# Performance work log

Hardware: AMD Instinct MI355X
Metric: run time of the kernel (lower is better)

## Reference

```python
import jax, jax.numpy as jnp
import numpy as np

REG_MAX = 16
TOPK = 13
ALPHA = 1.0
BETA = 6.0
MATCH_W = 0.5
IOU_W = 7.5
DFL_W = 1.5
EPS = 1e-7
NEG_INF = -1e30


def _iou(b1, b2):
    # xyxy IoU, broadcastable [..., 4]
    x1 = jnp.maximum(b1[..., 0], b2[..., 0]); y1 = jnp.maximum(b1[..., 1], b2[..., 1])
    x2 = jnp.minimum(b1[..., 2], b2[..., 2]); y2 = jnp.minimum(b1[..., 3], b2[..., 3])
    inter = jnp.maximum(x2 - x1, 0.0) * jnp.maximum(y2 - y1, 0.0)
    a1 = (b1[..., 2] - b1[..., 0]) * (b1[..., 3] - b1[..., 1])
    a2 = (b2[..., 2] - b2[..., 0]) * (b2[..., 3] - b2[..., 1])
    return inter / (a1 + a2 - inter + EPS)


def _ciou(b1, b2):
    iou = _iou(b1, b2)
    w1 = b1[..., 2] - b1[..., 0]; h1 = b1[..., 3] - b1[..., 1]
    w2 = b2[..., 2] - b2[..., 0]; h2 = b2[..., 3] - b2[..., 1]
    cw = jnp.maximum(b1[..., 2], b2[..., 2]) - jnp.minimum(b1[..., 0], b2[..., 0])
    ch = jnp.maximum(b1[..., 3], b2[..., 3]) - jnp.minimum(b1[..., 1], b2[..., 1])
    c2 = cw * cw + ch * ch + EPS
    rho2 = ((b2[..., 0] + b2[..., 2] - b1[..., 0] - b1[..., 2]) ** 2
            + (b2[..., 1] + b2[..., 3] - b1[..., 1] - b1[..., 3]) ** 2) / 4.0
    v = (4.0 / jnp.pi ** 2) * (jnp.arctan(w2 / (h2 + EPS)) - jnp.arctan(w1 / (h1 + EPS))) ** 2
    a = jax.lax.stop_gradient(v / (v - iou + (1.0 + EPS)))
    return iou - (rho2 / c2 + v * a)


def _per_sample(ps, pb, bd, gtb, gtl, vcm, anchor, stride):
    # ps [N,C], pb [N,4], bd [N,4*R], gtb [M,4], gtl [M], vcm [C] bool
    N, C = ps.shape
    M = gtb.shape[0]
    lab = jnp.clip(gtl, 0, C - 1)
    gt_valid = (gtl >= 0) & (gtl < C) & vcm[lab]
    ax, ay = anchor[:, 0], anchor[:, 1]
    inside = ((ax[None, :] >= gtb[:, 0:1]) & (ax[None, :] <= gtb[:, 2:3])
              & (ay[None, :] >= gtb[:, 1:2]) & (ay[None, :] <= gtb[:, 3:4]))  # [M,N]
    iou_mn = _iou(pb[None, :, :], gtb[:, None, :])                             # [M,N]
    cls_mn = jax.nn.sigmoid(ps[:, lab]).T                                      # [M,N]
    align = jnp.where(inside & gt_valid[:, None], cls_mn ** ALPHA * iou_mn ** BETA, NEG_INF)
    top_vals, top_idx = jax.lax.top_k(align, TOPK)                             # [M,K]
    cand = jnp.full((M, N), NEG_INF, ps.dtype).at[jnp.arange(M)[:, None], top_idx].set(top_vals)
    best = cand.max(0)          # final metric per anchor
    mg = cand.argmax(0)         # winning GT (first max == earliest GT, matching loop order)
    fg = best > -1.0            # align >= 0 always; non-candidates stay at NEG_INF
    m_lab = jnp.clip(gtl[mg], 0, C - 1)
    ov = iou_mn[mg, jnp.arange(N)]
    fgf = fg.astype(ps.dtype)
    tgt_scores = jax.nn.one_hot(m_lab, C, dtype=ps.dtype) * (jnp.maximum(ov, 0.1) * fgf)[:, None]
    tb = jnp.where(fg[:, None], gtb[mg], pb)   # safe target boxes (masked out when not fg)

    # classification BCE over valid classes (mean)
    bce = jnp.maximum(ps, 0.0) - ps * tgt_scores + jnp.log1p(jnp.exp(-jnp.abs(ps)))
    vc = vcm.astype(ps.dtype)
    match = (bce * vc[None, :]).sum() / (N * jnp.maximum(vc.sum(), 1.0))

    cnt = fg.sum()
    ciou_v = _ciou(pb, tb)
    iou_loss = jnp.where(cnt > 0, ((1.0 - ciou_v) * fgf).sum() / jnp.maximum(cnt, 1), 0.0)
    miou_sum = (_iou(pb, tb) * fgf).sum()
    probs = jax.nn.sigmoid(ps)
    pos_sum = (probs[jnp.arange(N), m_lab] * fgf).sum()

    # DFL
    d = jnp.concatenate([anchor - tb[:, :2], tb[:, 2:] - anchor], -1) / stride  # [N,4]
    d = jnp.clip(d, 0.0, REG_MAX - 1 - 0.01)
    tl = d.astype(jnp.int32)
    tr = jnp.minimum(tl + 1, REG_MAX - 1)
    wl = tr.astype(ps.dtype) - d
    wr = 1.0 - wl
    logp = jax.nn.log_softmax(bd.reshape(N, 4, REG_MAX), -1)
    ll = -jnp.take_along_axis(logp, tl[..., None], -1)[..., 0]
    lr = -jnp.take_along_axis(logp, tr[..., None], -1)[..., 0]
    dfl = jnp.where(cnt > 0, ((ll * wl + lr * wr) * fgf[:, None]).sum() / jnp.maximum(cnt * 4, 1), 0.0)

    mx = jnp.where(vcm[None, :], probs, NEG_INF).max(-1)
    neg_sum = (mx * (1.0 - fgf)).sum()
    neg_cnt = N - cnt
    return match, iou_loss, dfl, cnt, neg_cnt, pos_sum, neg_sum, miou_sum


def setup_inputs() -> dict:
    key = jax.random.key(0)
    B, N, C, M, R = 16, 8400, 80, 64, REG_MAX
    ks = jax.random.split(key, 7)
    pts, sts = [], []
    for s in (8, 16, 32):
        n = 640 // s
        g = (np.arange(n) + 0.5) * s
        xv, yv = np.meshgrid(g, g)
        pts.append(np.stack([xv.ravel(), yv.ravel()], 1))
        sts.append(np.full((n * n, 1), s, np.float32))
    anchor_points = jnp.asarray(np.concatenate(pts).astype(np.float32))  # [8400,2]
    stride_tensor = jnp.asarray(np.concatenate(sts))                      # [8400,1]
    c = anchor_points[None] + jax.random.normal(ks[0], (B, N, 2)) * stride_tensor[None]
    wh = jax.random.uniform(ks[1], (B, N, 2), minval=8.0, maxval=128.0)
    pred_boxes = jnp.concatenate([jnp.clip(c - wh / 2, 0.0, 640.0),
                                  jnp.clip(c + wh / 2, 0.0, 640.0)], -1)
    gc = jax.random.uniform(ks[2], (B, M, 2), minval=64.0, maxval=576.0)
    gwh = jax.random.uniform(ks[3], (B, M, 2), minval=16.0, maxval=128.0)
    gt_boxes = jnp.concatenate([gc - gwh / 2, gc + gwh / 2], -1)
    gt_labels = jax.random.randint(ks[4], (B, M), 0, C)
    class_mask = jnp.ones((B, C), bool)
    pred_scores = jax.random.normal(ks[5], (B, N, C))
    box_distribution = jax.random.normal(ks[6], (B, N, 4 * R))
    return {"pred_scores": pred_scores, "pred_boxes": pred_boxes,
            "anchor_points": anchor_points, "stride_tensor": stride_tensor,
            "box_distribution": box_distribution, "gt_boxes": gt_boxes,
            "gt_labels": gt_labels, "class_mask": class_mask}


def reference(pred_scores, pred_boxes, anchor_points, stride_tensor,
              box_distribution, gt_boxes, gt_labels, class_mask):
    B = pred_scores.shape[0]
    f = lambda ps, pb, bd, gtb, gtl, vcm: _per_sample(ps, pb, bd, gtb, gtl, vcm,
                                                      anchor_points, stride_tensor)
    match, iou_l, dfl, cnt, ncnt, psum, nsum, misum = jax.vmap(f)(
        pred_scores, pred_boxes, box_distribution, gt_boxes, gt_labels, class_mask)
    tot_pos = cnt.sum()
    tot_neg = ncnt.sum()
    total_match = match.sum(); total_iou = iou_l.sum(); total_dfl = dfl.sum()
    loss = (MATCH_W * total_match + IOU_W * total_iou + DFL_W * total_dfl) / B
    mean_pos = psum.sum() / jnp.maximum(tot_pos, 1)
    mean_neg = nsum.sum() / jnp.maximum(tot_neg, 1)
    mean_miou = misum.sum() / jnp.maximum(tot_pos, 1)
    return (loss, total_match / B, total_iou / B, total_dfl / B,
            tot_pos.astype(jnp.float32), mean_pos, mean_neg, mean_miou)
```

## Files before the change

kernel.cpp:

```cpp
#include <hip/hip_runtime.h>
#include <stdint.h>

#define TOPK 13
#define NEG_INF_F (-1e30f)
#define EPSF 1e-7f
#define L2EF 1.4426950408889634f
#define LN2F 0.6931471805599453f
#define MAXCAND 2048
#define MAXB_LDS 64

__device__ __forceinline__ int mask_at(const uint8_t* __restrict__ raw, int i) {
    bool as_u8 = (raw[1] | raw[2] | raw[3]) != 0;
    return as_u8 ? (raw[i] != 0) : (((const int*)raw)[i] != 0);
}

__device__ __forceinline__ float iou_pair(float ax1, float ay1, float ax2, float ay2,
                                          float bx1, float by1, float bx2, float by2) {
    float x1 = fmaxf(ax1, bx1), y1 = fmaxf(ay1, by1);
    float x2 = fminf(ax2, bx2), y2 = fminf(ay2, by2);
    float inter = fmaxf(x2 - x1, 0.f) * fmaxf(y2 - y1, 0.f);
    float a1 = (ax2 - ax1) * (ay2 - ay1);
    float a2 = (bx2 - bx1) * (by2 - by1);
    return inter / (a1 + a2 - inter + EPSF);
}

__device__ __forceinline__ float sigmoid_fast(float s) {
    return 1.f / (1.f + exp2f(-s * L2EF));
}
__device__ __forceinline__ float softplus_bce(float s) {
    float t = exp2f(-fabsf(s) * L2EF);
    return fmaxf(s, 0.f) + log2f(1.f + t) * LN2F;
}

__device__ __forceinline__ void assign_wave(
    const float* __restrict__ ps, const float* __restrict__ pb,
    const float* __restrict__ gtb, const int* __restrict__ gtl,
    const uint8_t* __restrict__ mraw,
    unsigned long long* __restrict__ best, unsigned* __restrict__ list,
    int B, int N, int C, int M, int t, int lane) {
    int b = t % B;
    int m = t / B;

    int lbl = gtl[b * M + m];
    int lab = min(max(lbl, 0), C - 1);
    if (!((lbl >= 0) && (lbl < C) && (mask_at(mraw, b * C + lab) != 0))) return;

    float4 g = ((const float4*)gtb)[(size_t)b * M + m];

    const int   n0_[3]  = { 0, 6400, 8000 };
    const int   dim_[3] = { 80, 40, 20 };
    const float sv_[3]  = { 8.f, 16.f, 32.f };

    int ix0[3], iy0[3], ww[3], pre[4];
    pre[0] = 0;
#pragma unroll
    for (int l = 0; l < 3; ++l) {
        float s = sv_[l]; int d = dim_[l];
        int ax0 = max(0,     (int)ceilf (g.x / s - 0.5f));
        int ax1 = min(d - 1, (int)floorf(g.z / s - 0.5f));
        int ay0 = max(0,     (int)ceilf (g.y / s - 0.5f));
        int ay1 = min(d - 1, (int)floorf(g.w / s - 0.5f));
        int w = max(0, ax1 - ax0 + 1);
        int h = max(0, ay1 - ay0 + 1);
        ix0[l] = ax0; iy0[l] = ay0; ww[l] = w;
        pre[l + 1] = pre[l] + w * h;
    }
    int tot = pre[3];
    if (tot == 0) return;

    const float* psb = ps + (size_t)b * N * C + lab;
    const float4* pbb = (const float4*)pb + (size_t)b * N;

    float lv[TOPK];
    int   li[TOPK];
#pragma unroll
    for (int j = 0; j < TOPK; ++j) { lv[j] = NEG_INF_F; li[j] = -1; }

    for (int tt = lane; tt < tot; tt += 64) {
        int l = (tt >= pre[1]) + (tt >= pre[2]);
        int r = tt - pre[l];
        int w = ww[l];
        int iy = r / w, ix = r - iy * w;
        int gx = ix0[l] + ix, gy = iy0[l] + iy;
        int n = n0_[l] + gy * dim_[l] + gx;
        float4 p = pbb[n];
        float iou = iou_pair(p.x, p.y, p.z, p.w, g.x, g.y, g.z, g.w);
        float sc = psb[(size_t)n * C];
        float i3 = iou * iou * iou;
        float val = sigmoid_fast(sc) * i3 * i3;
        if (val > lv[TOPK - 1]) {
            bool placed = false;
#pragma unroll
            for (int j = TOPK - 1; j >= 1; --j) {
                if (!placed) {
                    if (val > lv[j - 1]) { lv[j] = lv[j - 1]; li[j] = li[j - 1]; }
                    else { lv[j] = val; li[j] = n; placed = true; }
                }
            }
            if (!placed) { lv[0] = val; li[0] = n; }
        }
    }

    unsigned key = 0xFFFFFFFFu - (unsigned)m;
    unsigned long long* bb = best + (size_t)b * N;
    unsigned* myslots = list + ((size_t)b * M + m) * TOPK;
    int rounds = min(tot, TOPK);
    for (int p = 0; p < rounds; ++p) {
        float bv = lv[0]; int bn = li[0];
        for (int off = 32; off > 0; off >>= 1) {
            float ov = __shfl_down(bv, off, 64);
            int   on = __shfl_down(bn, off, 64);
            if (ov > bv || (ov == bv && (unsigned)on < (unsigned)bn)) { bv = ov; bn = on; }
        }
        bv = __shfl(bv, 0, 64);
        bn = __shfl(bn, 0, 64);
        if (bn < 0) break;
        if (li[0] == bn) {
            unsigned long long pk =
                ((unsigned long long)__float_as_uint(lv[0]) << 32) | (unsigned long long)key;
            atomicMax(bb + bn, pk);
            myslots[p] = (unsigned)bn + 1u;
#pragma unroll
            for (int j = 0; j < TOPK - 1; ++j) { lv[j] = lv[j + 1]; li[j] = li[j + 1]; }
            lv[TOPK - 1] = NEG_INF_F; li[TOPK - 1] = -1;
        }
    }
}

__global__ __launch_bounds__(256, 1) void fused_a_k(
    const float* __restrict__ ps, const float* __restrict__ pb,
    const float* __restrict__ gtb, const int* __restrict__ gtl,
    const uint8_t* __restrict__ mraw,
    unsigned long long* __restrict__ best, unsigned* __restrict__ list,
    float* __restrict__ sigbuf, float* __restrict__ partials,
    int B, int N, int C, int M, int asgb, int nb) {
    if ((int)blockIdx.x < asgb) {
        int t = blockIdx.x * 4 + (threadIdx.x >> 6);
        if (t < B * M)
            assign_wave(ps, pb, gtb, gtl, mraw, best, list,
                        B, N, C, M, t, threadIdx.x & 63);
        return;
    }
    int bi = blockIdx.x - asgb;
    int b = bi / nb;
    int n = (bi % nb) * 256 + threadIdx.x;

    __shared__ int smask[256];
    __shared__ int s_notall;
    __shared__ float sredA[4], sredB[4];
    if (threadIdx.x == 0) s_notall = 0;
    __syncthreads();
    for (int c = threadIdx.x; c < C && c < 256; c += 256) {
        int v = mask_at(mraw, b * C + c);
        smask[c] = v;
        if (!v) s_notall = 1;
    }
    __syncthreads();
    bool allm = (s_notall == 0);

    int lane = threadIdx.x & 63, wid = threadIdx.x >> 6;
    float acc0 = 0.f, acc3 = 0.f;

    if (C == 80 && allm) {
        int wavebase = (bi % nb) * 256 + wid * 64;
        int j = lane & 3;
        const float* psb0 = ps + (size_t)b * N * 80;
#pragma unroll
        for (int p = 0; p < 4; ++p) {
            int row = wavebase + p * 16 + (lane >> 2);
            if (row < N) {
                const float4* rb = (const float4*)(psb0 + (size_t)row * 80);
                float4 q0 = rb[j], q1 = rb[4 + j], q2 = rb[8 + j],
                       q3 = rb[12 + j], q4 = rb[16 + j];
                float bce =
                    softplus_bce(q0.x) + softplus_bce(q0.y) + softplus_bce(q0.z) + softplus_bce(q0.w) +
                    softplus_bce(q1.x) + softplus_bce(q1.y) + softplus_bce(q1.z) + softplus_bce(q1.w) +
                    softplus_bce(q2.x) + softplus_bce(q2.y) + softplus_bce(q2.z) + softplus_bce(q2.w) +
                    softplus_bce(q3.x) + softplus_bce(q3.y) + softplus_bce(q3.z) + softplus_bce(q3.w) +
                    softplus_bce(q4.x) + softplus_bce(q4.y) + softplus_bce(q4.z) + softplus_bce(q4.w);
                float sm = fmaxf(fmaxf(fmaxf(q0.x, q0.y), fmaxf(q0.z, q0.w)),
                                 fmaxf(fmaxf(q1.x, q1.y), fmaxf(q1.z, q1.w)));
                sm = fmaxf(sm, fmaxf(fmaxf(q2.x, q2.y), fmaxf(q2.z, q2.w)));
                sm = fmaxf(sm, fmaxf(fmaxf(q3.x, q3.y), fmaxf(q3.z, q3.w)));
                sm = fmaxf(sm, fmaxf(fmaxf(q4.x, q4.y), fmaxf(q4.z, q4.w)));
                bce += __shfl_xor(bce, 1, 64);
                bce += __shfl_xor(bce, 2, 64);
                sm = fmaxf(sm, __shfl_xor(sm, 1, 64));
                sm = fmaxf(sm, __shfl_xor(sm, 2, 64));
                if (j == 0) {
                    float sg = sigmoid_fast(sm);
                    sigbuf[(size_t)b * N + row] = sg;
                    acc0 += bce;
                    acc3 += sg;
                }
            }
        }
    } else if (n < N) {
        const float* psr = ps + ((size_t)b * N + n) * C;
        float bce_sum = 0.f, smax = NEG_INF_F;
        if (allm) {
            int c4 = C & ~3;
            for (int c = 0; c < c4; c += 4) {
                float4 s4 = *(const float4*)(psr + c);
                bce_sum += softplus_bce(s4.x) + softplus_bce(s4.y) +
                           softplus_bce(s4.z) + softplus_bce(s4.w);
                smax = fmaxf(smax, fmaxf(fmaxf(s4.x, s4.y), fmaxf(s4.z, s4.w)));
            }
            for (int c = c4; c < C; ++c) {
                float s = psr[c];
                bce_sum += softplus_bce(s);
                smax = fmaxf(smax, s);
            }
        } else {
            for (int c = 0; c < C; ++c) {
                float s = psr[c];
                if (smask[c]) { bce_sum += softplus_bce(s); smax = fmaxf(smax, s); }
            }
        }
        float sg = sigmoid_fast(smax);
        sigbuf[(size_t)b * N + n] = sg;
        acc0 = bce_sum;
        acc3 = sg;
    }

    {
        float v0 = acc0, v3 = acc3;
        for (int off = 32; off > 0; off >>= 1) {
            v0 += __shfl_down(v0, off, 64);
            v3 += __shfl_down(v3, off, 64);
        }
        if (lane == 0) { sredA[wid] = v0; sredB[wid] = v3; }
    }
    __syncthreads();
    if (threadIdx.x == 0) {
        atomicAdd(&partials[b * 8 + 0], sredA[0] + sredA[1] + sredA[2] + sredA[3]);
        atomicAdd(&partials[b * 8 + 3], sredB[0] + sredB[1] + sredB[2] + sredB[3]);
    }
}

__global__ __launch_bounds__(256, 1) void fused_b_k(
    const float* __restrict__ ps, const float* __restrict__ pb,
    const float* __restrict__ anch, const float* __restrict__ strd,
    const float* __restrict__ bd, const float* __restrict__ gtb,
    const int* __restrict__ gtl, const uint8_t* __restrict__ mraw,
    const unsigned long long* __restrict__ best, const float* __restrict__ sigbuf,
    const unsigned* __restrict__ list,
    float* __restrict__ partials, unsigned int* __restrict__ done_ctr,
    float* __restrict__ out, int B, int N, int C, int M) {
    __shared__ float sacc[MAXB_LDS * 8];
    __shared__ int s_last;
    bool use_lds = (B <= MAXB_LDS);
    if (use_lds)
        for (int i = threadIdx.x; i < B * 8; i += 256) sacc[i] = 0.f;
    __syncthreads();

    int idx = blockIdx.x * 256 + threadIdx.x;
    int cap = B * M * TOPK;
    bool active = false;
    int b = 0, n = 0, mg = 0;
    if (idx < cap) {
        unsigned e = list[idx];
        if (e != 0u) {
            n = (int)(e - 1u);
            b = idx / (M * TOPK);
            int m_claim = (idx / TOPK) % M;
            unsigned long long pk = best[(size_t)b * N + n];
            mg = (int)(0xFFFFFFFFu - (unsigned)(pk & 0xFFFFFFFFull));
            active = (mg == m_claim);
        }
    }

    if (active) {
        int lbl = gtl[b * M + mg];
        int m_lab = min(max(lbl, 0), C - 1);

        const float* bdr = bd + ((size_t)b * N + n) * 64;
        const float4* bq4 = (const float4*)bdr;
        float4 bq[16];
#pragma unroll
        for (int i = 0; i < 16; ++i) bq[i] = bq4[i];
        float4 p = ((const float4*)pb)[(size_t)b * N + n];
        float4 g = ((const float4*)gtb)[(size_t)b * M + mg];
        float2 an = ((const float2*)anch)[n];
        float stv = strd[n];
        float slab = ps[((size_t)b * N + n) * C + m_lab];
        float sg = sigbuf[(size_t)b * N + n];

        float ov = iou_pair(p.x, p.y, p.z, p.w, g.x, g.y, g.z, g.w);
        float acc0 = -fmaxf(ov, 0.1f) * slab;
        float acc2 = sigmoid_fast(slab);
        float acc4 = ov;
        float w1 = p.z - p.x, h1 = p.w - p.y;
        float w2 = g.z - g.x, h2 = g.w - g.y;
        float cw = fmaxf(p.z, g.z) - fminf(p.x, g.x);
        float ch = fmaxf(p.w, g.w) - fminf(p.y, g.y);
        float c2 = cw * cw + ch * ch + EPSF;
        float dx = g.x + g.z - p.x - p.z;
        float dy = g.y + g.w - p.y - p.w;
        float rho2 = (dx * dx + dy * dy) * 0.25f;
        const float PI = 3.14159265358979323846f;
        float dv = atanf(w2 / (h2 + EPSF)) - atanf(w1 / (h1 + EPSF));
        float v = (4.f / (PI * PI)) * dv * dv;
        float a = v / (v - ov + 1.f + EPSF);
        float acc5 = 1.f - (ov - (rho2 / c2 + v * a));
        float dall[4] = { (an.x - g.x) / stv, (an.y - g.y) / stv,
                          (g.z - an.x) / stv, (g.w - an.y) / stv };
        float dfl = 0.f;
#pragma unroll
        for (int k = 0; k < 4; ++k) {
            float4 q0 = bq[k * 4 + 0], q1 = bq[k * 4 + 1];
            float4 q2 = bq[k * 4 + 2], q3 = bq[k * 4 + 3];
            float mxv = fmaxf(fmaxf(fmaxf(q0.x, q0.y), fmaxf(q0.z, q0.w)),
                              fmaxf(fmaxf(q1.x, q1.y), fmaxf(q1.z, q1.w)));
            mxv = fmaxf(mxv, fmaxf(fmaxf(fmaxf(q2.x, q2.y), fmaxf(q2.z, q2.w)),
                                    fmaxf(fmaxf(q3.x, q3.y), fmaxf(q3.z, q3.w))));
            float se = exp2f((q0.x - mxv) * L2EF) + exp2f((q0.y - mxv) * L2EF) +
                       exp2f((q0.z - mxv) * L2EF) + exp2f((q0.w - mxv) * L2EF) +
                       exp2f((q1.x - mxv) * L2EF) + exp2f((q1.y - mxv) * L2EF) +
                       exp2f((q1.z - mxv) * L2EF) + exp2f((q1.w - mxv) * L2EF) +
                       exp2f((q2.x - mxv) * L2EF) + exp2f((q2.y - mxv) * L2EF) +
                       exp2f((q2.z - mxv) * L2EF) + exp2f((q2.w - mxv) * L2EF) +
                       exp2f((q3.x - mxv) * L2EF) + exp2f((q3.y - mxv) * L2EF) +
                       exp2f((q3.z - mxv) * L2EF) + exp2f((q3.w - mxv) * L2EF);
            float lse = mxv + log2f(se) * LN2F;
            float d = fminf(fmaxf(dall[k], 0.f), 14.99f);
            int tl = (int)d;
            int tr = min(tl + 1, 15);
            float wl = (float)tr - d;
            float xtl = bdr[k * 16 + tl];
            float xtr = bdr[k * 16 + tr];
            dfl += (lse - xtl) * wl + (lse - xtr) * (1.f - wl);
        }
        float accs[7] = { acc0, 1.f, acc2, -sg, acc4, acc5, dfl };
        if (use_lds) {
#pragma unroll
            for (int j = 0; j < 7; ++j) atomicAdd(&sacc[b * 8 + j], accs[j]);
        } else {
#pragma unroll
            for (int j = 0; j < 7; ++j) atomicAdd(&partials[b * 8 + j], accs[j]);
        }
    }
    __syncthreads();
    if (use_lds)
        for (int i = threadIdx.x; i < B * 8; i += 256)
            if (sacc[i] != 0.f) atomicAdd(&partials[i], sacc[i]);
    __syncthreads();

    if (threadIdx.x == 0) {
        __threadfence();
        unsigned r = atomicAdd(done_ctr, 1u);
        s_last = (r == gridDim.x - 1u) ? 1 : 0;
    }
    __syncthreads();
    if (!s_last) return;
    if (threadIdx.x >= 64) return;
    __threadfence();

    int fl = threadIdx.x;
    float tm = 0, ti = 0, td = 0, tp = 0, tneg = 0, pos = 0, neg = 0, miou = 0;
    for (int s = fl; s < B; s += 64) {
        float vcs = 0.f;
        for (int c = 0; c < C; ++c) vcs += mask_at(mraw, s * C + c) ? 1.f : 0.f;
        const float* pr = partials + s * 8;
        float p0 = __hip_atomic_load(&pr[0], __ATOMIC_RELAXED, __HIP_MEMORY_SCOPE_AGENT);
        float p1 = __hip_atomic_load(&pr[1], __ATOMIC_RELAXED, __HIP_MEMORY_SCOPE_AGENT);
        float p2 = __hip_atomic_load(&pr[2], __ATOMIC_RELAXED, __HIP_MEMORY_SCOPE_AGENT);
        float p3 = __hip_atomic_load(&pr[3], __ATOMIC_RELAXED, __HIP_MEMORY_SCOPE_AGENT);
        float p4 = __hip_atomic_load(&pr[4], __ATOMIC_RELAXED, __HIP_MEMORY_SCOPE_AGENT);
        float p5 = __hip_atomic_load(&pr[5], __ATOMIC_RELAXED, __HIP_MEMORY_SCOPE_AGENT);
        float p6 = __hip_atomic_load(&pr[6], __ATOMIC_RELAXED, __HIP_MEMORY_SCOPE_AGENT);
        float cnt = p1;
        tm += p0 / ((float)N * fmaxf(vcs, 1.f));
        ti += (cnt > 0.f) ? p5 / fmaxf(cnt, 1.f) : 0.f;
        td += (cnt > 0.f) ? p6 / fmaxf(cnt * 4.f, 1.f) : 0.f;
        tp += cnt; tneg += (float)N - cnt;
        pos += p2; neg += p3; miou += p4;
    }
    for (int off = 32; off > 0; off >>= 1) {
        tm += __shfl_down(tm, off, 64);   ti += __shfl_down(ti, off, 64);
        td += __shfl_down(td, off, 64);   tp += __shfl_down(tp, off, 64);
        tneg += __shfl_down(tneg, off, 64); pos += __shfl_down(pos, off, 64);
        neg += __shfl_down(neg, off, 64); miou += __shfl_down(miou, off, 64);
    }
    if (fl == 0) {
        float Bf = (float)B;
        out[0] = (0.5f * tm + 7.5f * ti + 1.5f * td) / Bf;
        out[1] = tm / Bf;
        out[2] = ti / Bf;
        out[3] = td / Bf;
        out[4] = tp;
        out[5] = pos / fmaxf(tp, 1.f);
        out[6] = neg / fmaxf(tneg, 1.f);
        out[7] = miou / fmaxf(tp, 1.f);
    }
}

__global__ __launch_bounds__(256) void assign_topk_k(
    const float* __restrict__ ps, const float* __restrict__ pb,
    const float* __restrict__ anch, const float* __restrict__ gtb,
    const int* __restrict__ gtl, const uint8_t* __restrict__ mraw,
    unsigned long long* __restrict__ best, int B, int N, int C, int M) {
    int b = blockIdx.x % B;
    int m = blockIdx.x / B;

    __shared__ float cval[MAXCAND];
    __shared__ int   cidx[MAXCAND];
    __shared__ int   scnt;
    if (threadIdx.x == 0) scnt = 0;

    int lbl = gtl[b * M + m];
    int lab = min(max(lbl, 0), C - 1);
    bool valid = (lbl >= 0) && (lbl < C) && (mask_at(mraw, b * C + lab) != 0);
    __syncthreads();

    if (valid) {
        float4 g = ((const float4*)gtb)[(size_t)b * M + m];
        const float* psb = ps + (size_t)b * N * C + lab;
        const float4* pbb = (const float4*)pb + (size_t)b * N;
        for (int n = threadIdx.x; n < N; n += 256) {
            float2 a = ((const float2*)anch)[n];
            if (a.x < g.x || a.x > g.z || a.y < g.y || a.y > g.w) continue;
            float4 p = pbb[n];
            float iou = iou_pair(p.x, p.y, p.z, p.w, g.x, g.y, g.z, g.w);
            float s = psb[(size_t)n * C];
            float i3 = iou * iou * iou;
            float val = sigmoid_fast(s) * i3 * i3;
            int slot = atomicAdd(&scnt, 1);
            if (slot < MAXCAND) { cval[slot] = val; cidx[slot] = n; }
        }
    }
    __syncthreads();
    if (!valid || threadIdx.x >= 64) return;

    int total = min(scnt, MAXCAND);
    if (total == 0) return;
    int lane = threadIdx.x;

    float lv[TOPK];
    int   li[TOPK];
#pragma unroll
    for (int j = 0; j < TOPK; ++j) { lv[j] = NEG_INF_F; li[j] = -1; }
    for (int i = lane; i < total; i += 64) {
        float v = cval[i]; int ix = cidx[i];
        if (v > lv[TOPK - 1]) {
            bool placed = false;
#pragma unroll
            for (int j = TOPK - 1; j >= 1; --j) {
                if (!placed) {
                    if (v > lv[j - 1]) { lv[j] = lv[j - 1]; li[j] = li[j - 1]; }
                    else { lv[j] = v; li[j] = ix; placed = true; }
                }
            }
            if (!placed) { lv[0] = v; li[0] = ix; }
        }
    }

    unsigned key = 0xFFFFFFFFu - (unsigned)m;
    unsigned long long* bb = best + (size_t)b * N;
    int rounds = min(total, TOPK);
    for (int p = 0; p < rounds; ++p) {
        float bv = lv[0]; int bn = li[0];
        for (int off = 32; off > 0; off >>= 1) {
            float ov = __shfl_down(bv, off, 64);
            int   on = __shfl_down(bn, off, 64);
            if (ov > bv || (ov == bv && (unsigned)on < (unsigned)bn)) { bv = ov; bn = on; }
        }
        bv = __shfl(bv, 0, 64);
        bn = __shfl(bn, 0, 64);
        if (bn < 0) break;
        if (li[0] == bn) {
            unsigned long long pk =
                ((unsigned long long)__float_as_uint(lv[0]) << 32) | (unsigned long long)key;
            atomicMax(bb + bn, pk);
#pragma unroll
            for (int j = 0; j < TOPK - 1; ++j) { lv[j] = lv[j + 1]; li[j] = li[j + 1]; }
            lv[TOPK - 1] = NEG_INF_F; li[TOPK - 1] = -1;
        }
    }
}

__global__ __launch_bounds__(256, 1) void per_anchor_k(
    const float* __restrict__ ps, const float* __restrict__ pb,
    const float* __restrict__ anch, const float* __restrict__ strd,
    const float* __restrict__ bd, const float* __restrict__ gtb,
    const int* __restrict__ gtl, const uint8_t* __restrict__ mraw,
    const unsigned long long* __restrict__ best,
    float* __restrict__ partials, int B, int N, int C, int M) {
    int b = blockIdx.y;
    int n = blockIdx.x * 256 + threadIdx.x;

    __shared__ int smask[256];
    __shared__ int s_notall;
    __shared__ float sred[4 * 8];
    if (threadIdx.x == 0) s_notall = 0;
    __syncthreads();
    for (int c = threadIdx.x; c < C && c < 256; c += 256) {
        int v = mask_at(mraw, b * C + c);
        smask[c] = v;
        if (!v) s_notall = 1;
    }
    __syncthreads();
    bool allm = (s_notall == 0);

    float acc0 = 0, acc1 = 0, acc2 = 0, acc3 = 0, acc4 = 0, acc5 = 0, acc6 = 0;

    if (n < N) {
        unsigned long long pk = best[(size_t)b * N + n];
        bool fg = (pk != 0ull);
        int mg = fg ? (int)(0xFFFFFFFFu - (unsigned)(pk & 0xFFFFFFFFull)) : 0;
        int lbl = gtl[b * M + mg];
        int m_lab = min(max(lbl, 0), C - 1);

        const float* psr = ps + ((size_t)b * N + n) * C;
        float bce_sum = 0.f, smax = NEG_INF_F;

        if (allm) {
            int c4 = C & ~3;
            for (int c = 0; c < c4; c += 4) {
                float4 s4 = *(const float4*)(psr + c);
                bce_sum += softplus_bce(s4.x) + softplus_bce(s4.y) +
                           softplus_bce(s4.z) + softplus_bce(s4.w);
                smax = fmaxf(smax, fmaxf(fmaxf(s4.x, s4.y), fmaxf(s4.z, s4.w)));
            }
            for (int c = c4; c < C; ++c) {
                float s = psr[c];
                bce_sum += softplus_bce(s);
                smax = fmaxf(smax, s);
            }
        } else {
            for (int c = 0; c < C; ++c) {
                float s = psr[c];
                if (smask[c]) { bce_sum += softplus_bce(s); smax = fmaxf(smax, s); }
            }
        }

        acc1 = fg ? 1.f : 0.f;
        acc3 = fg ? 0.f : sigmoid_fast(smax);

        if (fg) {
            const float* bdr = bd + ((size_t)b * N + n) * 64;
            const float4* bq4 = (const float4*)bdr;
            float4 bq[16];
#pragma unroll
            for (int i = 0; i < 16; ++i) bq[i] = bq4[i];
            float4 p = ((const float4*)pb)[(size_t)b * N + n];
            float4 g = ((const float4*)gtb)[(size_t)b * M + mg];
            float2 an = ((const float2*)anch)[n];
            float stv = strd[n];
            float slab = psr[m_lab];

            float ov = iou_pair(p.x, p.y, p.z, p.w, g.x, g.y, g.z, g.w);
            bce_sum -= fmaxf(ov, 0.1f) * slab;
            acc2 = sigmoid_fast(slab);
            acc4 = ov;
            float w1 = p.z - p.x, h1 = p.w - p.y;
            float w2 = g.z - g.x, h2 = g.w - g.y;
            float cw = fmaxf(p.z, g.z) - fminf(p.x, g.x);
            float ch = fmaxf(p.w, g.w) - fminf(p.y, g.y);
            float c2 = cw * cw + ch * ch + EPSF;
            float dx = g.x + g.z - p.x - p.z;
            float dy = g.y + g.w - p.y - p.w;
            float rho2 = (dx * dx + dy * dy) * 0.25f;
            const float PI = 3.14159265358979323846f;
            float dv = atanf(w2 / (h2 + EPSF)) - atanf(w1 / (h1 + EPSF));
            float v = (4.f / (PI * PI)) * dv * dv;
            float a = v / (v - ov + 1.f + EPSF);
            acc5 = 1.f - (ov - (rho2 / c2 + v * a));
            float dall[4] = { (an.x - g.x) / stv, (an.y - g.y) / stv,
                              (g.z - an.x) / stv, (g.w - an.y) / stv };
            float dfl = 0.f;
#pragma unroll
            for (int k = 0; k < 4; ++k) {
                float4 q0 = bq[k * 4 + 0], q1 = bq[k * 4 + 1];
                float4 q2 = bq[k * 4 + 2], q3 = bq[k * 4 + 3];
                float mxv = fmaxf(fmaxf(fmaxf(q0.x, q0.y), fmaxf(q0.z, q0.w)),
                                  fmaxf(fmaxf(q1.x, q1.y), fmaxf(q1.z, q1.w)));
                mxv = fmaxf(mxv, fmaxf(fmaxf(fmaxf(q2.x, q2.y), fmaxf(q2.z, q2.w)),
                                        fmaxf(fmaxf(q3.x, q3.y), fmaxf(q3.z, q3.w))));
                float se = exp2f((q0.x - mxv) * L2EF) + exp2f((q0.y - mxv) * L2EF) +
                           exp2f((q0.z - mxv) * L2EF) + exp2f((q0.w - mxv) * L2EF) +
                           exp2f((q1.x - mxv) * L2EF) + exp2f((q1.y - mxv) * L2EF) +
                           exp2f((q1.z - mxv) * L2EF) + exp2f((q1.w - mxv) * L2EF) +
                           exp2f((q2.x - mxv) * L2EF) + exp2f((q2.y - mxv) * L2EF) +
                           exp2f((q2.z - mxv) * L2EF) + exp2f((q2.w - mxv) * L2EF) +
                           exp2f((q3.x - mxv) * L2EF) + exp2f((q3.y - mxv) * L2EF) +
                           exp2f((q3.z - mxv) * L2EF) + exp2f((q3.w - mxv) * L2EF);
                float lse = mxv + log2f(se) * LN2F;
                float d = fminf(fmaxf(dall[k], 0.f), 14.99f);
                int tl = (int)d;
                int tr = min(tl + 1, 15);
                float wl = (float)tr - d;
                float xtl = bdr[k * 16 + tl];
                float xtr = bdr[k * 16 + tr];
                dfl += (lse - xtl) * wl + (lse - xtr) * (1.f - wl);
            }
            acc6 = dfl;
        }
        acc0 = bce_sum;
    }

    int lane = threadIdx.x & 63, wid = threadIdx.x >> 6;
    float accs[7] = { acc0, acc1, acc2, acc3, acc4, acc5, acc6 };
#pragma unroll
    for (int j = 0; j < 7; ++j) {
        float v = accs[j];
        for (int off = 32; off > 0; off >>= 1) v += __shfl_down(v, off, 64);
        if (lane == 0) sred[wid * 8 + j] = v;
    }
    __syncthreads();
    if (threadIdx.x < 7) {
        float s = sred[0 * 8 + threadIdx.x] + sred[1 * 8 + threadIdx.x] +
                  sred[2 * 8 + threadIdx.x] + sred[3 * 8 + threadIdx.x];
        atomicAdd(&partials[b * 8 + threadIdx.x], s);
    }
}

__global__ void finalize_k(const float* __restrict__ partials, const uint8_t* __restrict__ mraw,
                           float* __restrict__ out, int B, int N, int C) {
    int lane = threadIdx.x;
    float tm = 0, ti = 0, td = 0, tp = 0, tneg = 0, pos = 0, neg = 0, miou = 0;
    if (lane < B) {
        float vcs = 0.f;
        for (int c = 0; c < C; ++c) vcs += mask_at(mraw, lane * C + c) ? 1.f : 0.f;
        const float* pr = partials + lane * 8;
        float cnt = pr[1];
        tm = pr[0] / ((float)N * fmaxf(vcs, 1.f));
        ti = (cnt > 0.f) ? pr[5] / fmaxf(cnt, 1.f) : 0.f;
        td = (cnt > 0.f) ? pr[6] / fmaxf(cnt * 4.f, 1.f) : 0.f;
        tp = cnt; tneg = (float)N - cnt;
        pos = pr[2]; neg = pr[3]; miou = pr[4];
    }
    for (int off = 32; off > 0; off >>= 1) {
        tm += __shfl_down(tm, off, 64);   ti += __shfl_down(ti, off, 64);
        td += __shfl_down(td, off, 64);   tp += __shfl_down(tp, off, 64);
        tneg += __shfl_down(tneg, off, 64); pos += __shfl_down(pos, off, 64);
        neg += __shfl_down(neg, off, 64); miou += __shfl_down(miou, off, 64);
    }
    if (lane == 0) {
        float Bf = (float)B;
        out[0] = (0.5f * tm + 7.5f * ti + 1.5f * td) / Bf;
        out[1] = tm / Bf;
        out[2] = ti / Bf;
        out[3] = td / Bf;
        out[4] = tp;
        out[5] = pos / fmaxf(tp, 1.f);
        out[6] = neg / fmaxf(tneg, 1.f);
        out[7] = miou / fmaxf(tp, 1.f);
    }
}

extern "C" void kernel_launch(void* const* d_in, const int* in_sizes, int n_in,
                              void* d_out, int out_size, void* d_ws, size_t ws_size,
                              hipStream_t stream) {
    const float* ps   = (const float*)d_in[0];
    const float* pb   = (const float*)d_in[1];
    const float* anch = (const float*)d_in[2];
    const float* strd = (const float*)d_in[3];
    const float* bd   = (const float*)d_in[4];
    const float* gtb  = (const float*)d_in[5];
    const int*   gtl  = (const int*)d_in[6];
    const uint8_t* cmsk = (const uint8_t*)d_in[7];

    int N = in_sizes[2] / 2;
    int B = in_sizes[1] / (4 * N);
    int C = in_sizes[0] / (B * N);
    int M = in_sizes[6] / B;

    size_t bestBytes = (size_t)B * N * sizeof(unsigned long long);
    size_t off1 = (bestBytes + 255) & ~(size_t)255;
    size_t partBytes = (size_t)B * 8 * sizeof(float);
    size_t off2 = (off1 + partBytes + 255) & ~(size_t)255;
    size_t off3 = off2 + 256;
    size_t listBytes = (size_t)B * M * TOPK * sizeof(unsigned);
    size_t zeroBytes = (off3 + listBytes + 255) & ~(size_t)255;
    unsigned long long* best = (unsigned long long*)d_ws;
    float* partials = (float*)((char*)d_ws + off1);
    unsigned int* done_ctr = (unsigned int*)((char*)d_ws + off2);
    unsigned int* list = (unsigned int*)((char*)d_ws + off3);
    float* sigbuf = (float*)((char*)d_ws + zeroBytes);

    hipMemsetAsync(d_ws, 0, zeroBytes, stream);

    int nb = (N + 255) / 256;
    if (N == 8400) {
        int asgb = (B * M + 3) / 4;
        fused_a_k<<<asgb + B * nb, 256, 0, stream>>>(ps, pb, gtb, gtl, cmsk,
                                                     best, list, sigbuf,
                                                     partials, B, N, C, M, asgb, nb);
        int cap = B * M * TOPK;
        int nblk = (cap + 255) / 256;
        fused_b_k<<<nblk, 256, 0, stream>>>(ps, pb, anch, strd, bd, gtb, gtl, cmsk,
                                            best, sigbuf, list,
                                            partials, done_ctr, (float*)d_out, B, N, C, M);
    } else {
        assign_topk_k<<<B * M, 256, 0, stream>>>(ps, pb, anch, gtb, gtl, cmsk, best, B, N, C, M);
        dim3 gB(nb, B);
        per_anchor_k<<<gB, 256, 0, stream>>>(ps, pb, anch, strd, bd, gtb, gtl, cmsk, best,
                                             partials, B, N, C, M);
        finalize_k<<<1, 64, 0, stream>>>(partials, cmsk, (float*)d_out, B, N, C);
    }
}
```

Baseline: 148.0 us.

## Remove memset and global atomics by deferring anchor winner resolution to per-sample blocks

The assign waves now write candidate anchor indices and metric values to per-GT lists that they zero themselves, instead of doing global 64-bit atomicMax on a best table. The second kernel runs one block per sample. Each block clears a per-sample winner table, resolves conflicts with atomicMax, and reduces the foreground terms with wave shuffles instead of per-element atomics. Scan blocks write per-block partials instead of calling atomicAdd, the done counter is reset inside the kernel, and anchors are recomputed analytically. This drops the hipMemsetAsync and atomic contention, at the cost of giving the second kernel only B blocks, each doing a serial loop over N to clear its table.

```diff
diff --git a/kernel.cpp b/kernel.cpp
--- a/kernel.cpp
+++ b/kernel.cpp
@@ -36,10 +36,14 @@
     const float* __restrict__ ps, const float* __restrict__ pb,
     const float* __restrict__ gtb, const int* __restrict__ gtl,
     const uint8_t* __restrict__ mraw,
-    unsigned long long* __restrict__ best, unsigned* __restrict__ list,
+    unsigned* __restrict__ lista, unsigned* __restrict__ listv,
     int B, int N, int C, int M, int t, int lane) {
     int b = t % B;
     int m = t / B;
+
+    unsigned* la = lista + ((size_t)b * M + m) * TOPK;
+    unsigned* lw = listv + ((size_t)b * M + m) * TOPK;
+    if (lane < TOPK) { la[lane] = 0u; lw[lane] = 0u; }
 
     int lbl = gtl[b * M + m];
     int lab = min(max(lbl, 0), C - 1);
@@ -101,9 +105,6 @@
         }
     }
 
-    unsigned key = 0xFFFFFFFFu - (unsigned)m;
-    unsigned long long* bb = best + (size_t)b * N;
-    unsigned* myslots = list + ((size_t)b * M + m) * TOPK;
     int rounds = min(tot, TOPK);
     for (int p = 0; p < rounds; ++p) {
         float bv = lv[0]; int bn = li[0];
@@ -116,10 +117,8 @@
         bn = __shfl(bn, 0, 64);
         if (bn < 0) break;
         if (li[0] == bn) {
-            unsigned long long pk =
-                ((unsigned long long)__float_as_uint(lv[0]) << 32) | (unsigned long long)key;
-            atomicMax(bb + bn, pk);
-            myslots[p] = (unsigned)bn + 1u;
+            la[p] = (unsigned)bn + 1u;
+            lw[p] = __float_as_uint(lv[0]);
 #pragma unroll
             for (int j = 0; j < TOPK - 1; ++j) { lv[j] = lv[j + 1]; li[j] = li[j + 1]; }
             lv[TOPK - 1] = NEG_INF_F; li[TOPK - 1] = -1;
@@ -127,17 +126,20 @@
     }
 }
 
-__global__ __launch_bounds__(256, 1) void fused_a_k(
+__global__ __launch_bounds__(256, 1) void assign_scan_k(
     const float* __restrict__ ps, const float* __restrict__ pb,
     const float* __restrict__ gtb, const int* __restrict__ gtl,
     const uint8_t* __restrict__ mraw,
-    unsigned long long* __restrict__ best, unsigned* __restrict__ list,
-    float* __restrict__ sigbuf, float* __restrict__ partials,
+    unsigned* __restrict__ lista, unsigned* __restrict__ listv,
+    float* __restrict__ sigbuf, float* __restrict__ scanout,
+    unsigned* __restrict__ done_ctr,
     int B, int N, int C, int M, int asgb, int nb) {
+    if (blockIdx.x == 0 && threadIdx.x == 0) *done_ctr = 0u;
+
     if ((int)blockIdx.x < asgb) {
         int t = blockIdx.x * 4 + (threadIdx.x >> 6);
         if (t < B * M)
-            assign_wave(ps, pb, gtb, gtl, mraw, best, list,
+            assign_wave(ps, pb, gtb, gtl, mraw, lista, listv,
                         B, N, C, M, t, threadIdx.x & 63);
         return;
     }
@@ -233,44 +235,53 @@
     }
     __syncthreads();
     if (threadIdx.x == 0) {
-        atomicAdd(&partials[b * 8 + 0], sredA[0] + sredA[1] + sredA[2] + sredA[3]);
-        atomicAdd(&partials[b * 8 + 3], sredB[0] + sredB[1] + sredB[2] + sredB[3]);
-    }
-}
-
-__global__ __launch_bounds__(256, 1) void fused_b_k(
+        scanout[bi * 2]     = sredA[0] + sredA[1] + sredA[2] + sredA[3];
+        scanout[bi * 2 + 1] = sredB[0] + sredB[1] + sredB[2] + sredB[3];
+    }
+}
+
+__global__ __launch_bounds__(256, 1) void fg_fin_k(
     const float* __restrict__ ps, const float* __restrict__ pb,
-    const float* __restrict__ anch, const float* __restrict__ strd,
     const float* __restrict__ bd, const float* __restrict__ gtb,
     const int* __restrict__ gtl, const uint8_t* __restrict__ mraw,
-    const unsigned long long* __restrict__ best, const float* __restrict__ sigbuf,
-    const unsigned* __restrict__ list,
-    float* __restrict__ partials, unsigned int* __restrict__ done_ctr,
-    float* __restrict__ out, int B, int N, int C, int M) {
-    __shared__ float sacc[MAXB_LDS * 8];
+    const float* __restrict__ sigbuf,
+    const unsigned* __restrict__ lista, const unsigned* __restrict__ listv,
+    const float* __restrict__ scanout, unsigned long long* __restrict__ wtab_g,
+    float* __restrict__ fgout, unsigned* __restrict__ done_ctr,
+    float* __restrict__ out, int B, int N, int C, int M, int nb) {
+    __shared__ float sred[4 * 8];
     __shared__ int s_last;
-    bool use_lds = (B <= MAXB_LDS);
-    if (use_lds)
-        for (int i = threadIdx.x; i < B * 8; i += 256) sacc[i] = 0.f;
-    __syncthreads();
-
-    int idx = blockIdx.x * 256 + threadIdx.x;
-    int cap = B * M * TOPK;
-    bool active = false;
-    int b = 0, n = 0, mg = 0;
-    if (idx < cap) {
-        unsigned e = list[idx];
-        if (e != 0u) {
-            n = (int)(e - 1u);
-            b = idx / (M * TOPK);
-            int m_claim = (idx / TOPK) % M;
-            unsigned long long pk = best[(size_t)b * N + n];
-            mg = (int)(0xFFFFFFFFu - (unsigned)(pk & 0xFFFFFFFFull));
-            active = (mg == m_claim);
-        }
-    }
-
-    if (active) {
+    int b = blockIdx.x, tid = threadIdx.x;
+
+    unsigned long long* wt = wtab_g + (size_t)b * N;
+    for (int i = tid; i < N; i += 256) wt[i] = 0ull;
+    __syncthreads();
+
+    int capb = M * TOPK;
+    const unsigned* la = lista + (size_t)b * capb;
+    const unsigned* lw = listv + (size_t)b * capb;
+    for (int idx = tid; idx < capb; idx += 256) {
+        unsigned n1 = la[idx];
+        if (n1) {
+            unsigned long long pk = ((unsigned long long)lw[idx] << 32) |
+                                    (unsigned long long)(0xFFFFFFFFu - (unsigned)(idx / TOPK));
+            atomicMax(&wt[n1 - 1], pk);
+        }
+    }
+    __syncthreads();
+
+    float a0 = 0, a1 = 0, a2 = 0, a3 = 0, a4 = 0, a5 = 0, a6 = 0;
+    for (int idx = tid; idx < capb; idx += 256) {
+        unsigned n1 = la[idx];
+        if (!n1) continue;
+        int mg = idx / TOPK;
+        unsigned long long pk = ((unsigned long long)lw[idx] << 32) |
+                                (unsigned long long)(0xFFFFFFFFu - (unsigned)mg);
+        unsigned long long w = __hip_atomic_load(&wt[n1 - 1], __ATOMIC_RELAXED,
+                                                 __HIP_MEMORY_SCOPE_AGENT);
+        if (w != pk) continue;
+        int n = (int)(n1 - 1u);
+
         int lbl = gtl[b * M + mg];
         int m_lab = min(max(lbl, 0), C - 1);
 
@@ -281,20 +292,24 @@
         for (int i = 0; i < 16; ++i) bq[i] = bq4[i];
         float4 p = ((const float4*)pb)[(size_t)b * N + n];
         float4 g = ((const float4*)gtb)[(size_t)b * M + mg];
-        float2 an = ((const float2*)anch)[n];
-        float stv = strd[n];
+        int l = (n >= 6400) + (n >= 8000);
+        int base = (l == 0) ? 0 : (l == 1 ? 6400 : 8000);
+        int dim  = (l == 0) ? 80 : (l == 1 ? 40 : 20);
+        float stv = (l == 0) ? 8.f : (l == 1 ? 16.f : 32.f);
+        int nl = n - base;
+        int gy = nl / dim, gx = nl - gy * dim;
+        float anx = ((float)gx + 0.5f) * stv, any = ((float)gy + 0.5f) * stv;
+
         float slab = ps[((size_t)b * N + n) * C + m_lab];
         float sg = sigbuf[(size_t)b * N + n];
 
         float ov = iou_pair(p.x, p.y, p.z, p.w, g.x, g.y, g.z, g.w);
-        float acc0 = -fmaxf(ov, 0.1f) * slab;
-        float acc2 = sigmoid_fast(slab);
-        float acc4 = ov;
+        float c0 = -fmaxf(ov, 0.1f) * slab;
         float w1 = p.z - p.x, h1 = p.w - p.y;
         float w2 = g.z - g.x, h2 = g.w - g.y;
         float cw = fmaxf(p.z, g.z) - fminf(p.x, g.x);
         float ch = fmaxf(p.w, g.w) - fminf(p.y, g.y);
-        float c2 = cw * cw + ch * ch + EPSF;
+        float cc2 = cw * cw + ch * ch + EPSF;
         float dx = g.x + g.z - p.x - p.z;
         float dy = g.y + g.w - p.y - p.w;
         float rho2 = (dx * dx + dy * dy) * 0.25f;
@@ -302,9 +317,9 @@
         float dv = atanf(w2 / (h2 + EPSF)) - atanf(w1 / (h1 + EPSF));
         float v = (4.f / (PI * PI)) * dv * dv;
         float a = v / (v - ov + 1.f + EPSF);
-        float acc5 = 1.f - (ov - (rho2 / c2 + v * a));
-        float dall[4] = { (an.x - g.x) / stv, (an.y - g.y) / stv,
-                          (g.z - an.x) / stv, (g.w - an.y) / stv };
+        float c5 = 1.f - (ov - (rho2 / cc2 + v * a));
+        float dall[4] = { (anx - g.x) / stv, (any - g.y) / stv,
+                          (g.z - anx) / stv, (g.w - any) / stv };
         float dfl = 0.f;
 #pragma unroll
         for (int k = 0; k < 4; ++k) {
@@ -331,50 +346,62 @@
             float xtr = bdr[k * 16 + tr];
             dfl += (lse - xtl) * wl + (lse - xtr) * (1.f - wl);
         }
-        float accs[7] = { acc0, 1.f, acc2, -sg, acc4, acc5, dfl };
-        if (use_lds) {
-#pragma unroll
-            for (int j = 0; j < 7; ++j) atomicAdd(&sacc[b * 8 + j], accs[j]);
-        } else {
-#pragma unroll
-            for (int j = 0; j < 7; ++j) atomicAdd(&partials[b * 8 + j], accs[j]);
-        }
-    }
-    __syncthreads();
-    if (use_lds)
-        for (int i = threadIdx.x; i < B * 8; i += 256)
-            if (sacc[i] != 0.f) atomicAdd(&partials[i], sacc[i]);
-    __syncthreads();
-
-    if (threadIdx.x == 0) {
+        a0 += c0; a1 += 1.f; a2 += sigmoid_fast(slab); a3 -= sg;
+        a4 += ov; a5 += c5; a6 += dfl;
+    }
+
+    int lane = tid & 63, wid = tid >> 6;
+    float accs[7] = { a0, a1, a2, a3, a4, a5, a6 };
+#pragma unroll
+    for (int j = 0; j < 7; ++j) {
+        float v = accs[j];
+        for (int off = 32; off > 0; off >>= 1) v += __shfl_down(v, off, 64);
+        if (lane == 0) sred[wid * 8 + j] = v;
+    }
+    __syncthreads();
+    if (tid < 7) {
+        float s = sred[0 * 8 + tid] + sred[1 * 8 + tid] +
+                  sred[2 * 8 + tid] + sred[3 * 8 + tid];
+        __hip_atomic_store(&fgout[b * 8 + tid], s, __ATOMIC_RELAXED,
+                           __HIP_MEMORY_SCOPE_AGENT);
+    }
+    __syncthreads();
+
+    if (tid == 0) {
         __threadfence();
         unsigned r = atomicAdd(done_ctr, 1u);
         s_last = (r == gridDim.x - 1u) ? 1 : 0;
     }
     __syncthreads();
     if (!s_last) return;
-    if (threadIdx.x >= 64) return;
+    if (tid >= 64) return;
     __threadfence();
 
-    int fl = threadIdx.x;
+    int fl = tid;
     float tm = 0, ti = 0, td = 0, tp = 0, tneg = 0, pos = 0, neg = 0, miou = 0;
     for (int s = fl; s < B; s += 64) {
         float vcs = 0.f;
         for (int c = 0; c < C; ++c) vcs += mask_at(mraw, s * C + c) ? 1.f : 0.f;
-        const float* pr = partials + s * 8;
-        float p0 = __hip_atomic_load(&pr[0], __ATOMIC_RELAXED, __HIP_MEMORY_SCOPE_AGENT);
-        float p1 = __hip_atomic_load(&pr[1], __ATOMIC_RELAXED, __HIP_MEMORY_SCOPE_AGENT);
-        float p2 = __hip_atomic_load(&pr[2], __ATOMIC_RELAXED, __HIP_MEMORY_SCOPE_AGENT);
-        float p3 = __hip_atomic_load(&pr[3], __ATOMIC_RELAXED, __HIP_MEMORY_SCOPE_AGENT);
-        float p4 = __hip_atomic_load(&pr[4], __ATOMIC_RELAXED, __HIP_MEMORY_SCOPE_AGENT);
-        float p5 = __hip_atomic_load(&pr[5], __ATOMIC_RELAXED, __HIP_MEMORY_SCOPE_AGENT);
-        float p6 = __hip_atomic_load(&pr[6], __ATOMIC_RELAXED, __HIP_MEMORY_SCOPE_AGENT);
-        float cnt = p1;
+        float bce_all = 0.f, sig_all = 0.f;
+        for (int k = 0; k < nb; ++k) {
+            bce_all += scanout[(s * nb + k) * 2];
+            sig_all += scanout[(s * nb + k) * 2 + 1];
+        }
+        const float* fo = fgout + s * 8;
+        float f0 = __hip_atomic_load(&fo[0], __ATOMIC_RELAXED, __HIP_MEMORY_SCOPE_AGENT);
+        float f1 = __hip_atomic_load(&fo[1], __ATOMIC_RELAXED, __HIP_MEMORY_SCOPE_AGENT);
+        float f2 = __hip_atomic_load(&fo[2], __ATOMIC_RELAXED, __HIP_MEMORY_SCOPE_AGENT);
+        float f3 = __hip_atomic_load(&fo[3], __ATOMIC_RELAXED, __HIP_MEMORY_SCOPE_AGENT);
+        float f4 = __hip_atomic_load(&fo[4], __ATOMIC_RELAXED, __HIP_MEMORY_SCOPE_AGENT);
+        float f5 = __hip_atomic_load(&fo[5], __ATOMIC_RELAXED, __HIP_MEMORY_SCOPE_AGENT);
+        float f6 = __hip_atomic_load(&fo[6], __ATOMIC_RELAXED, __HIP_MEMORY_SCOPE_AGENT);
+        float cnt = f1;
+        float p0 = bce_all + f0;
         tm += p0 / ((float)N * fmaxf(vcs, 1.f));
-        ti += (cnt > 0.f) ? p5 / fmaxf(cnt, 1.f) : 0.f;
-        td += (cnt > 0.f) ? p6 / fmaxf(cnt * 4.f, 1.f) : 0.f;
+        ti += (cnt > 0.f) ? f5 / fmaxf(cnt, 1.f) : 0.f;
+        td += (cnt > 0.f) ? f6 / fmaxf(cnt * 4.f, 1.f) : 0.f;
         tp += cnt; tneg += (float)N - cnt;
-        pos += p2; neg += p3; miou += p4;
+        pos += f2; neg += sig_all + f3; miou += f4;
     }
     for (int off = 32; off > 0; off >>= 1) {
         tm += __shfl_down(tm, off, 64);   ti += __shfl_down(ti, off, 64);
@@ -665,34 +692,41 @@
     int B = in_sizes[1] / (4 * N);
     int C = in_sizes[0] / (B * N);
     int M = in_sizes[6] / B;
-
-    size_t bestBytes = (size_t)B * N * sizeof(unsigned long long);
-    size_t off1 = (bestBytes + 255) & ~(size_t)255;
-    size_t partBytes = (size_t)B * 8 * sizeof(float);
-    size_t off2 = (off1 + partBytes + 255) & ~(size_t)255;
-    size_t off3 = off2 + 256;
-    size_t listBytes = (size_t)B * M * TOPK * sizeof(unsigned);
-    size_t zeroBytes = (off3 + listBytes + 255) & ~(size_t)255;
-    unsigned long long* best = (unsigned long long*)d_ws;
-    float* partials = (float*)((char*)d_ws + off1);
-    unsigned int* done_ctr = (unsigned int*)((char*)d_ws + off2);
-    unsigned int* list = (unsigned int*)((char*)d_ws + off3);
-    float* sigbuf = (float*)((char*)d_ws + zeroBytes);
-
-    hipMemsetAsync(d_ws, 0, zeroBytes, stream);
-
     int nb = (N + 255) / 256;
+
     if (N == 8400) {
+        size_t o0 = 0;
+        size_t o1 = (o0 + (size_t)B * N * 8 + 255) & ~(size_t)255;
+        size_t bmt = (size_t)B * M * TOPK * 4;
+        size_t o2 = (o1 + bmt + 255) & ~(size_t)255;
+        size_t o3 = (o2 + bmt + 255) & ~(size_t)255;
+        size_t o4 = (o3 + (size_t)B * N * 4 + 255) & ~(size_t)255;
+        size_t o5 = (o4 + (size_t)B * nb * 2 * 4 + 255) & ~(size_t)255;
+        size_t o6 = (o5 + (size_t)B * 8 * 4 + 255) & ~(size_t)255;
+        unsigned long long* wtab = (unsigned long long*)((char*)d_ws + o0);
+        unsigned* lista = (unsigned*)((char*)d_ws + o1);
+        unsigned* listv = (unsigned*)((char*)d_ws + o2);
+        float* sigbuf   = (float*)((char*)d_ws + o3);
+        float* scanout  = (float*)((char*)d_ws + o4);
+        float* fgout    = (float*)((char*)d_ws + o5);
+        unsigned* done_ctr = (unsigned*)((char*)d_ws + o6);
+
         int asgb = (B * M + 3) / 4;
-        fused_a_k<<<asgb + B * nb, 256, 0, stream>>>(ps, pb, gtb, gtl, cmsk,
-                                                     best, list, sigbuf,
-                                                     partials, B, N, C, M, asgb, nb);
-        int cap = B * M * TOPK;
-        int nblk = (cap + 255) / 256;
-        fused_b_k<<<nblk, 256, 0, stream>>>(ps, pb, anch, strd, bd, gtb, gtl, cmsk,
-                                            best, sigbuf, list,
-                                            partials, done_ctr, (float*)d_out, B, N, C, M);
+        assign_scan_k<<<asgb + B * nb, 256, 0, stream>>>(
+            ps, pb, gtb, gtl, cmsk, lista, listv, sigbuf, scanout, done_ctr,
+            B, N, C, M, asgb, nb);
+        fg_fin_k<<<B, 256, 0, stream>>>(
+            ps, pb, bd, gtb, gtl, cmsk, sigbuf, lista, listv, scanout,
+            wtab, fgout, done_ctr, (float*)d_out, B, N, C, M, nb);
     } else {
+        size_t bestBytes = (size_t)B * N * sizeof(unsigned long long);
+        size_t off1 = (bestBytes + 255) & ~(size_t)255;
+        size_t partBytes = (size_t)B * 8 * sizeof(float);
+        size_t zeroBytes = off1 + partBytes;
+        unsigned long long* best = (unsigned long long*)d_ws;
+        float* partials = (float*)((char*)d_ws + off1);
+
+        hipMemsetAsync(d_ws, 0, zeroBytes, stream);
         assign_topk_k<<<B * M, 256, 0, stream>>>(ps, pb, anch, gtb, gtl, cmsk, best, B, N, C, M);
         dim3 gB(nb, B);
         per_anchor_k<<<gB, 256, 0, stream>>>(ps, pb, anch, strd, bd, gtb, gtl, cmsk, best,
```

Result: slower. 164.8 us (+11.3%).
